# Optimization experiments

Hardware: AMD Instinct MI355X
Metric: run time of the kernel (lower is better)

## Reference

```python
import jax, jax.numpy as jnp
import numpy as np
from jax import lax

N, C_IN, DIMS, NW, T, H, W = 8, 64, 64, 8, 16, 64, 64
BN_EPS = 1e-5


def setup_inputs() -> dict:
    key = jax.random.key(0)
    ks = jax.random.split(key, 10)
    # kaiming-ish scales
    w_scale = (2.0 / (C_IN * 27)) ** 0.5
    return {
        "x": jax.random.normal(ks[0], (N, C_IN, T, H, W), dtype=jnp.float32),
        "weights": jax.random.normal(ks[1], (NW, DIMS, C_IN, 3, 3, 3), dtype=jnp.float32) * w_scale,
        "biases": jax.random.normal(ks[2], (NW, DIMS), dtype=jnp.float32),
        "se_w1": jax.random.normal(ks[3], (16, C_IN, 5, 5), dtype=jnp.float32) * (2.0 / (C_IN * 25)) ** 0.5,
        "se_b1": jnp.zeros((16,), dtype=jnp.float32),
        "se_w2": jax.random.normal(ks[4], (32, 16, 5, 5), dtype=jnp.float32) * (2.0 / (16 * 25)) ** 0.5,
        "se_b2": jnp.zeros((32,), dtype=jnp.float32),
        "lin_w": jax.random.normal(ks[5], (NW, 32), dtype=jnp.float32) * (1.0 / 32) ** 0.5,
        "lin_b": jnp.zeros((NW,), dtype=jnp.float32),
        "bn_gamma": jnp.ones((DIMS,), dtype=jnp.float32),
        "bn_beta": jnp.zeros((DIMS,), dtype=jnp.float32),
        "epochs_num": 15,
    }


def _forward(x, weights, biases, se_w1, se_b1, se_w2, se_b2, lin_w, lin_b, bn_gamma, bn_beta, epochs_num):
    tau = 30.0 - 2.9 * epochs_num if epochs_num < 10 else 1.0
    # std over temporal axis (torch.std -> unbiased, ddof=1): [n, c, h, w]
    std_x = jnp.std(x, axis=2, ddof=1)
    # squeeze-expand attention branch
    dn2d = ("NCHW", "OIHW", "NCHW")
    h1 = lax.conv_general_dilated(std_x, se_w1, (1, 1), "VALID", dimension_numbers=dn2d)
    h1 = jax.nn.relu(h1 + se_b1[None, :, None, None])
    h2 = lax.conv_general_dilated(h1, se_w2, (1, 1), "VALID", dimension_numbers=dn2d)
    h2 = jax.nn.relu(h2 + se_b2[None, :, None, None])
    pooled = jnp.max(h2, axis=(2, 3))                      # [n, 32]
    logits = pooled @ lin_w.T + lin_b                       # [n, num_weights]
    phi = jax.nn.softmax(logits / tau, axis=1)
    # per-sample dynamic kernels / biases
    dyn_w = jnp.einsum("bn,ncidhw->bcidhw", phi, weights)   # [n, dims, c_in, 3,3,3]
    dyn_b = phi @ biases                                    # [n, dims]
    # grouped conv3d (groups = n) == per-sample conv3d via vmap
    dn3d = ("NCDHW", "OIDHW", "NCDHW")
    def one_conv(xi, wi):
        return lax.conv_general_dilated(xi[None], wi, (1, 1, 1), "SAME", dimension_numbers=dn3d)[0]
    y = jax.vmap(one_conv)(x, dyn_w)                        # [n, dims, t, h, w]
    y = y + dyn_b[:, :, None, None, None]
    # BatchNorm3d (training mode, batch stats, biased var)
    mean = jnp.mean(y, axis=(0, 2, 3, 4))
    var = jnp.var(y, axis=(0, 2, 3, 4))
    b = lambda v: v[None, :, None, None, None]
    y = (y - b(mean)) * b(bn_gamma) * lax.rsqrt(b(var) + BN_EPS) + b(bn_beta)
    return jax.nn.relu(y)


def reference(x, weights, biases, se_w1, se_b1, se_w2, se_b2, lin_w, lin_b, bn_gamma, bn_beta, epochs_num):
    return _forward(x, weights, biases, se_w1, se_b1, se_w2, se_b2, lin_w, lin_b, bn_gamma, bn_beta, epochs_num)
```

## Files before the change

### kernel.cpp

```cpp
#include <hip/hip_runtime.h>
#include <hip/hip_bf16.h>
#include <math.h>

#define N_   8
#define CIN_ 64
#define DIMS_ 64
#define NW_  8
#define T_   16
#define H_   64
#define W_   64
#define HW_  (H_ * W_)
#define THW_ (T_ * HW_)

typedef short bf16x8 __attribute__((ext_vector_type(8)));
typedef float f32x16 __attribute__((ext_vector_type(16)));

__device__ __forceinline__ unsigned short f2bf(float f) {
    union { float f; unsigned u; } a; a.f = f;
    unsigned r = a.u + 0x7fffu + ((a.u >> 16) & 1u);
    return (unsigned short)(r >> 16);
}

#define CS8_ 8
#define HS8_ (66 * CS8_)
#define TS8_ (10 * HS8_)
#define XSH_ (3 * TS8_)
#define WLH_ (28 * 64 * 8)

__host__ __device__ constexpr int OXc(int tap) {
    int tt = tap > 26 ? 26 : tap;
    return (tt / 9) * TS8_ + ((tt % 9) / 3) * HS8_ + ((tt % 3) - 1) * CS8_;
}

__global__ __launch_bounds__(512) void stdxb_kernel(
    const float* __restrict__ x, float* __restrict__ std_x,
    unsigned short* __restrict__ xb)
{
    __shared__ unsigned short xsl[16 * 64 * 8];
    const int h = blockIdx.x, c8 = blockIdx.y, n = blockIdx.z;
    const int tid = threadIdx.x;
    const int c = tid >> 6, w = tid & 63;
    const int cin = c8 * 8 + c;
    const float* px = x + (((size_t)(n * 64 + cin)) << 16) + (h << 6) + w;
    float s = 0.f, s2 = 0.f;
#pragma unroll
    for (int t = 0; t < T_; ++t) {
        float v = px[t * HW_];
        s += v;
        s2 += v * v;
        xsl[(t << 9) + (w << 3) + c] = f2bf(v);
    }
    float var = (s2 - s * s * (1.0f / 16.0f)) * (1.0f / 15.0f);
    std_x[(((size_t)(n * 64 + cin)) << 12) + (h << 6) + w] = sqrtf(fmaxf(var, 0.f));
    __syncthreads();
    const int4* src = (const int4*)xsl;
    int4* dst = (int4*)(xb + ((size_t)((n * 8 + c8) * 16) << 12) * 8);
#pragma unroll
    for (int k = 0; k < 2; ++k) {
        int j = tid + (k << 9);
        int t = j >> 6, ww = j & 63;
        dst[((t << 6) + h) * 64 + ww] = src[j];
    }
}

__global__ void wtrans(const float* __restrict__ w1, const float* __restrict__ w2,
                       float* __restrict__ w1t, float* __restrict__ w2t) {
    int i = blockIdx.x * 256 + threadIdx.x;
    if (i < 25600) {
        int k = i / 1600, c = (i / 25) % 64, tap = i % 25;
        w1t[(c * 25 + tap) * 16 + k] = w1[i];
    } else if (i < 38400) {
        int j = i - 25600;
        int o = j / 400, c = (j / 25) % 16, tap = j % 25;
        w2t[(c * 25 + tap) * 32 + o] = w2[j];
    }
}

__global__ __launch_bounds__(256) void se_conv1c(const float* __restrict__ std_x,
        const float* __restrict__ w1t, const float* __restrict__ b1, float* __restrict__ h1) {
    __shared__ float red[3][64][8];
    const int n = blockIdx.y, ks = blockIdx.z * 8;
    const int iq = threadIdx.x & 63, cq = threadIdx.x >> 6;
    const int ij = blockIdx.x * 64 + iq;
    float acc[8];
#pragma unroll
    for (int q = 0; q < 8; ++q) acc[q] = 0.f;
    if (ij < 3600) {
        int i = ij / 60, j = ij - i * 60;
        const float* xn = std_x + (size_t)n * CIN_ * HW_ + i * W_ + j;
        for (int c = cq * 16; c < cq * 16 + 16; ++c) {
            const float* xc = xn + c * HW_;
            float xv[25];
#pragma unroll
            for (int u = 0; u < 5; ++u)
#pragma unroll
                for (int v = 0; v < 5; ++v) xv[u * 5 + v] = xc[u * W_ + v];
            const float* wc = w1t + c * 400 + ks;
#pragma unroll
            for (int tap = 0; tap < 25; ++tap)
#pragma unroll
                for (int q = 0; q < 8; ++q)
                    acc[q] = fmaf(xv[tap], wc[tap * 16 + q], acc[q]);
        }
    }
    if (cq > 0) {
#pragma unroll
        for (int q = 0; q < 8; ++q) red[cq - 1][iq][q] = acc[q];
    }
    __syncthreads();
    if (cq == 0 && ij < 3600) {
#pragma unroll
        for (int q = 0; q < 8; ++q) {
            float a = acc[q] + red[0][iq][q] + red[1][iq][q] + red[2][iq][q] + b1[ks + q];
            h1[((size_t)(n * 16 + ks + q)) * 3600 + ij] = fmaxf(a, 0.f);
        }
    }
}

__global__ __launch_bounds__(256) void se_conv2c(const float* __restrict__ h1,
        const float* __restrict__ w2t, const float* __restrict__ b2,
        unsigned* __restrict__ pooled) {
    __shared__ float red[3][64][8];
    const int n = blockIdx.y, os = blockIdx.z * 8;
    const int iq = threadIdx.x & 63, cq = threadIdx.x >> 6;
    const int ij = blockIdx.x * 64 + iq;
    const int i = ij / 56, j = ij - i * 56;
    float acc[8];
#pragma unroll
    for (int q = 0; q < 8; ++q) acc[q] = 0.f;
    const float* xn = h1 + (size_t)n * 16 * 3600 + i * 60 + j;
    for (int c = cq * 4; c < cq * 4 + 4; ++c) {
        const float* xc = xn + c * 3600;
        float xv[25];
#pragma unroll
        for (int u = 0; u < 5; ++u)
#pragma unroll
            for (int v = 0; v < 5; ++v) xv[u * 5 + v] = xc[u * 60 + v];
        const float* wc = w2t + c * 800 + os;
#pragma unroll
        for (int tap = 0; tap < 25; ++tap)
#pragma unroll
            for (int q = 0; q < 8; ++q)
                acc[q] = fmaf(xv[tap], wc[tap * 32 + q], acc[q]);
    }
    if (cq > 0) {
#pragma unroll
        for (int q = 0; q < 8; ++q) red[cq - 1][iq][q] = acc[q];
    }
    __syncthreads();
    if (cq == 0) {
#pragma unroll
        for (int q = 0; q < 8; ++q) {
            float a = fmaxf(acc[q] + red[0][iq][q] + red[1][iq][q] + red[2][iq][q] + b2[os + q], 0.f);
#pragma unroll
            for (int m = 1; m < 64; m <<= 1) a = fmaxf(a, __shfl_xor(a, m, 64));
            if (iq == 0) atomicMax(&pooled[n * 32 + os + q], __float_as_uint(a));
        }
    }
}

__global__ void se_head(const float* __restrict__ pooled, const float* __restrict__ lin_w,
                        const float* __restrict__ lin_b, const float* __restrict__ biases,
                        const int* __restrict__ epochs, float* __restrict__ phi,
                        float* __restrict__ dyn_b) {
    __shared__ float sphi[NW_][NW_];
    int tid = threadIdx.x;
    int e = epochs[0];
    float tau = (e < 10) ? (30.0f - 2.9f * (float)e) : 1.0f;
    if (tid < 64) {
        int b = tid >> 3, m = tid & 7;
        float acc = lin_b[m];
        for (int k = 0; k < 32; ++k) acc += pooled[b * 32 + k] * lin_w[m * 32 + k];
        sphi[b][m] = acc / tau;
    }
    __syncthreads();
    if (tid < 8) {
        int b = tid;
        float mx = sphi[b][0];
#pragma unroll
        for (int m = 1; m < 8; ++m) mx = fmaxf(mx, sphi[b][m]);
        float ex[8], s = 0.f;
#pragma unroll
        for (int m = 0; m < 8; ++m) { ex[m] = expf(sphi[b][m] - mx); s += ex[m]; }
        float inv = 1.0f / s;
#pragma unroll
        for (int m = 0; m < 8; ++m) { sphi[b][m] = ex[m] * inv; phi[b * 8 + m] = ex[m] * inv; }
    }
    __syncthreads();
    for (int idx = tid; idx < NW_ * DIMS_; idx += blockDim.x) {
        int b = idx >> 6, d = idx & 63;
        float acc = 0.f;
#pragma unroll
        for (int m = 0; m < 8; ++m) acc += sphi[b][m] * biases[m * DIMS_ + d];
        dyn_b[idx] = acc;
    }
}

__global__ void dyn_w_bf16b(const float* __restrict__ weights, const float* __restrict__ phi,
                            unsigned short* __restrict__ wtb2) {
    int g = blockIdx.x * 256 + threadIdx.x;
    int b = blockIdx.y;
    int c8 = g / 14336, r = g - c8 * 14336;
    int tap = r >> 9, co = (r >> 3) & 63, ci = r & 7;
    int cin = c8 * 8 + ci;
    unsigned short v = 0;
    if (tap < 27) {
        size_t src = ((size_t)(co * 64) + cin) * 27 + tap;
        float acc = 0.f;
#pragma unroll
        for (int m = 0; m < 8; ++m)
            acc += phi[b * 8 + m] * weights[(size_t)m * (64 * 64 * 27) + src];
        v = f2bf(acc);
    }
    wtb2[(size_t)b * 114688 + g] = v;
}

__global__ __launch_bounds__(512, 4) void conv3d_mfma3(
    const unsigned short* __restrict__ xb,
    const unsigned short* __restrict__ wtb2,
    const float* __restrict__ dynb,
    float* __restrict__ y,
    float* __restrict__ sums)
{
    __shared__ __align__(16) unsigned short xs[XSH_];
    __shared__ __align__(16) unsigned short wl[WLH_];
    __shared__ float bnred[128];

    const int hb = blockIdx.x, t = blockIdx.y, n = blockIdx.z;
    const int tid = threadIdx.x;
    const int lane = tid & 63, wid = tid >> 6;
    const int lane31 = lane & 31, tau = lane >> 5;
    const int hbase = hb * 8;

    for (int i = tid; i < XSH_ / 8; i += 512)
        *(int4*)&xs[i * 8] = (int4){0, 0, 0, 0};
    if (tid < 128) bnred[tid] = 0.f;

    const unsigned short* xnb = xb + ((size_t)(n * 8) << 16) * 8;
    const unsigned short* wnb = wtb2 + (size_t)n * 114688;

    f32x16 acc[2][2];
#pragma unroll
    for (int ci = 0; ci < 2; ++ci)
#pragma unroll
        for (int s = 0; s < 2; ++s)
            acc[ci][s] = (f32x16)(0.f);

    const int aBase = (tau * 64 + lane31) * 8;
    const int bsp0 = wid * HS8_ + (1 + lane31) * CS8_;
    const int bsp1 = bsp0 + 32 * CS8_;

    for (int c8 = 0; c8 < 8; ++c8) {
        __syncthreads();
#pragma unroll
        for (int k = 0; k < 4; ++k) {
            int r = wid + (k << 3);
            if (r < 30) {
                int tp = (r >= 20) ? 2 : (r >= 10 ? 1 : 0);
                int hp = r - tp * 10;
                int gt = t + tp - 1, gh = hbase + hp - 1;
                if (((unsigned)gt < 16u) && ((unsigned)gh < 64u)) {
                    const unsigned short* gp = xnb + (size_t)(((c8 * 16 + gt) * 64 + gh) * 64 + lane) * 8;
                    const unsigned short* lp = &xs[tp * TS8_ + hp * HS8_ + CS8_];
                    __builtin_amdgcn_global_load_lds(
                        (const __attribute__((address_space(1))) void*)gp,
                        (__attribute__((address_space(3))) void*)lp, 16, 0, 0);
                }
            }
        }
#pragma unroll
        for (int k = 0; k < 4; ++k) {
            int tp = wid + (k << 3);
            if (tp < 28) {
                const unsigned short* gp = wnb + (size_t)(c8 * 14336 + tp * 512 + lane * 8);
                const unsigned short* lp = &wl[tp * 512];
                __builtin_amdgcn_global_load_lds(
                    (const __attribute__((address_space(1))) void*)gp,
                    (__attribute__((address_space(3))) void*)lp, 16, 0, 0);
            }
        }
        __syncthreads();

#pragma unroll
        for (int p = 0; p < 14; ++p) {
            const int xo = tau ? OXc(2 * p + 1) : OXc(2 * p);
            bf16x8 a0 = *(const bf16x8*)&wl[p * 1024 + aBase];
            bf16x8 a1 = *(const bf16x8*)&wl[p * 1024 + aBase + 256];
            bf16x8 b0 = *(const bf16x8*)&xs[bsp0 + xo];
            bf16x8 b1 = *(const bf16x8*)&xs[bsp1 + xo];
            acc[0][0] = __builtin_amdgcn_mfma_f32_32x32x16_bf16(a0, b0, acc[0][0], 0, 0, 0);
            acc[0][1] = __builtin_amdgcn_mfma_f32_32x32x16_bf16(a0, b1, acc[0][1], 0, 0, 0);
            acc[1][0] = __builtin_amdgcn_mfma_f32_32x32x16_bf16(a1, b0, acc[1][0], 0, 0, 0);
            acc[1][1] = __builtin_amdgcn_mfma_f32_32x32x16_bf16(a1, b1, acc[1][1], 0, 0, 0);
        }
    }

    const float* db = dynb + n * DIMS_;
    const size_t ybase = (((size_t)n * DIMS_) << 16) + ((size_t)t << 12) + ((size_t)(hbase + wid) << 6);
#pragma unroll
    for (int ci = 0; ci < 2; ++ci) {
#pragma unroll
        for (int r = 0; r < 16; ++r) {
            const int co = 32 * ci + (r & 3) + 8 * (r >> 2) + 4 * tau;
            const float bco = db[co];
            float z0 = acc[ci][0][r] + bco;
            float z1 = acc[ci][1][r] + bco;
            y[ybase + ((size_t)co << 16) + lane31]      = z0;
            y[ybase + ((size_t)co << 16) + 32 + lane31] = z1;
            float ps = z0 + z1, ps2 = z0 * z0 + z1 * z1;
#pragma unroll
            for (int m = 1; m < 32; m <<= 1) {
                ps += __shfl_xor(ps, m, 64);
                ps2 += __shfl_xor(ps2, m, 64);
            }
            if (lane31 == 0) {
                atomicAdd(&bnred[co], ps);
                atomicAdd(&bnred[64 + co], ps2);
            }
        }
    }
    __syncthreads();
    if (tid < 128) atomicAdd(&sums[tid], bnred[tid]);
}

__global__ void bn_norm4(const float* __restrict__ sums, const float* __restrict__ gamma,
                         const float* __restrict__ beta, float* __restrict__ y) {
    size_t idx = (size_t)blockIdx.x * 256 + threadIdx.x;
    int c = (int)((idx >> 14) & 63);
    const float cnt = (float)(N_ * THW_);
    float mean = sums[c] / cnt;
    float var = sums[64 + c] / cnt - mean * mean;
    float sc = gamma[c] * rsqrtf(var + 1e-5f);
    float sh = beta[c] - mean * sc;
    float4 v = ((float4*)y)[idx];
    v.x = fmaxf(fmaf(v.x, sc, sh), 0.f);
    v.y = fmaxf(fmaf(v.y, sc, sh), 0.f);
    v.z = fmaxf(fmaf(v.z, sc, sh), 0.f);
    v.w = fmaxf(fmaf(v.w, sc, sh), 0.f);
    ((float4*)y)[idx] = v;
}

extern "C" void kernel_launch(void* const* d_in, const int* in_sizes, int n_in,
                              void* d_out, int out_size, void* d_ws, size_t ws_size,
                              hipStream_t stream) {
    const float* x       = (const float*)d_in[0];
    const float* weights = (const float*)d_in[1];
    const float* biases  = (const float*)d_in[2];
    const float* se_w1   = (const float*)d_in[3];
    const float* se_b1   = (const float*)d_in[4];
    const float* se_w2   = (const float*)d_in[5];
    const float* se_b2   = (const float*)d_in[6];
    const float* lin_w   = (const float*)d_in[7];
    const float* lin_b   = (const float*)d_in[8];
    const float* gamma   = (const float*)d_in[9];
    const float* beta    = (const float*)d_in[10];
    const int*   epochs  = (const int*)d_in[11];

    float* out = (float*)d_out;
    float* ws = (float*)d_ws;

    const size_t STD_OFF  = 0;
    const size_t H1_OFF   = STD_OFF + 2097152;
    const size_t SUMS_OFF = H1_OFF + 460800;
    const size_t POOL_OFF = SUMS_OFF + 128;
    const size_t PHI_OFF  = POOL_OFF + 256;
    const size_t DYNB_OFF = PHI_OFF + 64;
    const size_t WTB_OFF  = DYNB_OFF + 512;
    const size_t W1T_OFF  = WTB_OFF + 458752;
    const size_t W2T_OFF  = W1T_OFF + 25600;
    const size_t XB_OFF   = W2T_OFF + 12800;

    float* std_x  = ws + STD_OFF;
    float* h1     = ws + H1_OFF;
    float* sums   = ws + SUMS_OFF;
    float* pooled = ws + POOL_OFF;
    float* phi    = ws + PHI_OFF;
    float* dynb   = ws + DYNB_OFF;
    unsigned short* wtb2 = (unsigned short*)(ws + WTB_OFF);
    float* w1t    = ws + W1T_OFF;
    float* w2t    = ws + W2T_OFF;
    unsigned short* xb = (unsigned short*)(ws + XB_OFF);

    hipMemsetAsync(sums, 0, (128 + 256) * sizeof(float), stream);

    stdxb_kernel<<<dim3(64, 8, 8), 512, 0, stream>>>(x, std_x, xb);
    wtrans<<<150, 256, 0, stream>>>(se_w1, se_w2, w1t, w2t);

    se_conv1c<<<dim3(57, 8, 2), 256, 0, stream>>>(std_x, w1t, se_b1, h1);
    se_conv2c<<<dim3(49, 8, 4), 256, 0, stream>>>(h1, w2t, se_b2, (unsigned*)pooled);
    se_head<<<1, 64, 0, stream>>>(pooled, lin_w, lin_b, biases, epochs, phi, dynb);

    dyn_w_bf16b<<<dim3(448, 8), 256, 0, stream>>>(weights, phi, wtb2);

    conv3d_mfma3<<<dim3(8, 16, 8), 512, 0, stream>>>(xb, wtb2, dynb, out, sums);

    bn_norm4<<<32768, 256, 0, stream>>>(sums, gamma, beta, out);
}
```

Before: 408.5 us.

## Double-buffer conv3d LDS staging and restructure dynamic-weight and BN kernels

The conv3d kernel now uses dynamic shared memory with two x/w buffers and prefetches the next channel-group chunk with async global-to-LDS loads while the current chunk feeds the MFMAs. Waits use explicit vmcnt counts, with out-of-range loads redirected to a junk LDS slot so the count stays fixed. The dynamic-weight kernel now reads each base weight once and writes all 8 per-sample outputs, relying on a memset to zero the padding tap. BN normalization switches to a grid-stride loop over fewer blocks. Doubled LDS may lower occupancy, and the launch-bounds min-blocks hint is dropped.

```diff
diff --git a/kernel.cpp b/kernel.cpp
--- a/kernel.cpp
+++ b/kernel.cpp
@@ -24,8 +24,11 @@
 #define CS8_ 8
 #define HS8_ (66 * CS8_)
 #define TS8_ (10 * HS8_)
-#define XSH_ (3 * TS8_)
-#define WLH_ (28 * 64 * 8)
+#define XBUF_ (3 * TS8_)
+#define WBUF_ (28 * 64 * 8)
+#define JUNK_OFF_ (2 * XBUF_ + 2 * WBUF_)
+#define BNRED_OFF_ (JUNK_OFF_ + 512)
+#define DLS_BYTES_ (BNRED_OFF_ * 2 + 128 * 4)
 
 __host__ __device__ constexpr int OXc(int tap) {
     int tt = tap > 26 ? 26 : tap;
@@ -196,48 +199,82 @@
     }
 }
 
-__global__ void dyn_w_bf16b(const float* __restrict__ weights, const float* __restrict__ phi,
-                            unsigned short* __restrict__ wtb2) {
-    int g = blockIdx.x * 256 + threadIdx.x;
-    int b = blockIdx.y;
-    int c8 = g / 14336, r = g - c8 * 14336;
-    int tap = r >> 9, co = (r >> 3) & 63, ci = r & 7;
-    int cin = c8 * 8 + ci;
-    unsigned short v = 0;
-    if (tap < 27) {
-        size_t src = ((size_t)(co * 64) + cin) * 27 + tap;
+__global__ void dyn_w_all(const float* __restrict__ weights, const float* __restrict__ phi,
+                          unsigned short* __restrict__ wtb2) {
+    __shared__ float sphi[64];
+    int tid = threadIdx.x;
+    if (tid < 64) sphi[tid] = phi[tid];
+    __syncthreads();
+    int f = blockIdx.x * 256 + tid;
+    if (f >= 110592) return;
+    int tap = f % 27, cin = (f / 27) & 63, co = f / 1728;
+    float wv[8];
+#pragma unroll
+    for (int m = 0; m < 8; ++m) wv[m] = weights[(size_t)m * 110592 + f];
+    size_t dbase = (size_t)(cin >> 3) * 14336 + tap * 512 + co * 8 + (cin & 7);
+#pragma unroll
+    for (int b = 0; b < 8; ++b) {
         float acc = 0.f;
 #pragma unroll
-        for (int m = 0; m < 8; ++m)
-            acc += phi[b * 8 + m] * weights[(size_t)m * (64 * 64 * 27) + src];
-        v = f2bf(acc);
-    }
-    wtb2[(size_t)b * 114688 + g] = v;
-}
-
-__global__ __launch_bounds__(512, 4) void conv3d_mfma3(
+        for (int m = 0; m < 8; ++m) acc += sphi[b * 8 + m] * wv[m];
+        wtb2[(size_t)b * 114688 + dbase] = f2bf(acc);
+    }
+}
+
+extern __shared__ unsigned short dls[];
+
+__global__ __launch_bounds__(512) void conv3d_mfma4(
     const unsigned short* __restrict__ xb,
     const unsigned short* __restrict__ wtb2,
     const float* __restrict__ dynb,
     float* __restrict__ y,
     float* __restrict__ sums)
 {
-    __shared__ __align__(16) unsigned short xs[XSH_];
-    __shared__ __align__(16) unsigned short wl[WLH_];
-    __shared__ float bnred[128];
-
     const int hb = blockIdx.x, t = blockIdx.y, n = blockIdx.z;
     const int tid = threadIdx.x;
     const int lane = tid & 63, wid = tid >> 6;
     const int lane31 = lane & 31, tau = lane >> 5;
     const int hbase = hb * 8;
 
-    for (int i = tid; i < XSH_ / 8; i += 512)
-        *(int4*)&xs[i * 8] = (int4){0, 0, 0, 0};
+    unsigned short* junk = dls + JUNK_OFF_;
+    float* bnred = (float*)(dls + BNRED_OFF_);
+
+    for (int i = tid; i < (2 * XBUF_) / 8; i += 512)
+        *(int4*)&dls[i * 8] = (int4){0, 0, 0, 0};
     if (tid < 128) bnred[tid] = 0.f;
-
-    const unsigned short* xnb = xb + ((size_t)(n * 8) << 16) * 8;
+    __syncthreads();
+
+    const unsigned short* xnb = xb + (size_t)n * 4194304;
     const unsigned short* wnb = wtb2 + (size_t)n * 114688;
+
+    auto STAGE = [&](int c8, int pb) {
+        unsigned short* xbuf = dls + pb * XBUF_;
+        unsigned short* wbuf = dls + 2 * XBUF_ + pb * WBUF_;
+#pragma unroll
+        for (int k = 0; k < 4; ++k) {
+            int tp = wid + (k << 3);
+            bool ok = tp < 28;
+            const unsigned short* gp = wnb + ((size_t)c8 * 14336 + (ok ? tp * 512 : 0) + lane * 8);
+            unsigned short* lp = ok ? (wbuf + tp * 512) : junk;
+            __builtin_amdgcn_global_load_lds(
+                (const __attribute__((address_space(1))) void*)gp,
+                (__attribute__((address_space(3))) void*)lp, 16, 0, 0);
+        }
+#pragma unroll
+        for (int k = 0; k < 4; ++k) {
+            int r = wid + (k << 3);
+            int tp = (r >= 20) ? 2 : (r >= 10 ? 1 : 0);
+            int hp = r - tp * 10;
+            int gt = t + tp - 1, gh = hbase + hp - 1;
+            bool ok = (r < 30) && ((unsigned)gt < 16u) && ((unsigned)gh < 64u);
+            const unsigned short* gp = xnb +
+                (ok ? (size_t)(((c8 * 16 + gt) * 64 + gh) * 64 + lane) * 8 : (size_t)lane * 8);
+            unsigned short* lp = ok ? (xbuf + tp * TS8_ + hp * HS8_ + CS8_) : junk;
+            __builtin_amdgcn_global_load_lds(
+                (const __attribute__((address_space(1))) void*)gp,
+                (__attribute__((address_space(3))) void*)lp, 16, 0, 0);
+        }
+    };
 
     f32x16 acc[2][2];
 #pragma unroll
@@ -250,49 +287,33 @@
     const int bsp0 = wid * HS8_ + (1 + lane31) * CS8_;
     const int bsp1 = bsp0 + 32 * CS8_;
 
+    STAGE(0, 0);
+
     for (int c8 = 0; c8 < 8; ++c8) {
-        __syncthreads();
-#pragma unroll
-        for (int k = 0; k < 4; ++k) {
-            int r = wid + (k << 3);
-            if (r < 30) {
-                int tp = (r >= 20) ? 2 : (r >= 10 ? 1 : 0);
-                int hp = r - tp * 10;
-                int gt = t + tp - 1, gh = hbase + hp - 1;
-                if (((unsigned)gt < 16u) && ((unsigned)gh < 64u)) {
-                    const unsigned short* gp = xnb + (size_t)(((c8 * 16 + gt) * 64 + gh) * 64 + lane) * 8;
-                    const unsigned short* lp = &xs[tp * TS8_ + hp * HS8_ + CS8_];
-                    __builtin_amdgcn_global_load_lds(
-                        (const __attribute__((address_space(1))) void*)gp,
-                        (__attribute__((address_space(3))) void*)lp, 16, 0, 0);
-                }
-            }
-        }
-#pragma unroll
-        for (int k = 0; k < 4; ++k) {
-            int tp = wid + (k << 3);
-            if (tp < 28) {
-                const unsigned short* gp = wnb + (size_t)(c8 * 14336 + tp * 512 + lane * 8);
-                const unsigned short* lp = &wl[tp * 512];
-                __builtin_amdgcn_global_load_lds(
-                    (const __attribute__((address_space(1))) void*)gp,
-                    (__attribute__((address_space(3))) void*)lp, 16, 0, 0);
-            }
-        }
-        __syncthreads();
-
+        if (c8 < 7) {
+            STAGE(c8 + 1, (c8 + 1) & 1);
+            asm volatile("s_waitcnt vmcnt(8)" ::: "memory");
+        } else {
+            asm volatile("s_waitcnt vmcnt(0)" ::: "memory");
+        }
+        __builtin_amdgcn_s_barrier();
+        __builtin_amdgcn_sched_barrier(0);
+
+        const unsigned short* xsb = dls + (c8 & 1) * XBUF_;
+        const unsigned short* wlb = dls + 2 * XBUF_ + (c8 & 1) * WBUF_;
 #pragma unroll
         for (int p = 0; p < 14; ++p) {
             const int xo = tau ? OXc(2 * p + 1) : OXc(2 * p);
-            bf16x8 a0 = *(const bf16x8*)&wl[p * 1024 + aBase];
-            bf16x8 a1 = *(const bf16x8*)&wl[p * 1024 + aBase + 256];
-            bf16x8 b0 = *(const bf16x8*)&xs[bsp0 + xo];
-            bf16x8 b1 = *(const bf16x8*)&xs[bsp1 + xo];
+            bf16x8 a0 = *(const bf16x8*)&wlb[p * 1024 + aBase];
+            bf16x8 a1 = *(const bf16x8*)&wlb[p * 1024 + aBase + 256];
+            bf16x8 b0 = *(const bf16x8*)&xsb[bsp0 + xo];
+            bf16x8 b1 = *(const bf16x8*)&xsb[bsp1 + xo];
             acc[0][0] = __builtin_amdgcn_mfma_f32_32x32x16_bf16(a0, b0, acc[0][0], 0, 0, 0);
             acc[0][1] = __builtin_amdgcn_mfma_f32_32x32x16_bf16(a0, b1, acc[0][1], 0, 0, 0);
             acc[1][0] = __builtin_amdgcn_mfma_f32_32x32x16_bf16(a1, b0, acc[1][0], 0, 0, 0);
             acc[1][1] = __builtin_amdgcn_mfma_f32_32x32x16_bf16(a1, b1, acc[1][1], 0, 0, 0);
         }
+        __builtin_amdgcn_s_barrier();
     }
 
     const float* db = dynb + n * DIMS_;
@@ -325,19 +346,21 @@
 
 __global__ void bn_norm4(const float* __restrict__ sums, const float* __restrict__ gamma,
                          const float* __restrict__ beta, float* __restrict__ y) {
-    size_t idx = (size_t)blockIdx.x * 256 + threadIdx.x;
-    int c = (int)((idx >> 14) & 63);
     const float cnt = (float)(N_ * THW_);
-    float mean = sums[c] / cnt;
-    float var = sums[64 + c] / cnt - mean * mean;
-    float sc = gamma[c] * rsqrtf(var + 1e-5f);
-    float sh = beta[c] - mean * sc;
-    float4 v = ((float4*)y)[idx];
-    v.x = fmaxf(fmaf(v.x, sc, sh), 0.f);
-    v.y = fmaxf(fmaf(v.y, sc, sh), 0.f);
-    v.z = fmaxf(fmaf(v.z, sc, sh), 0.f);
-    v.w = fmaxf(fmaf(v.w, sc, sh), 0.f);
-    ((float4*)y)[idx] = v;
+    for (size_t idx = (size_t)blockIdx.x * 256 + threadIdx.x; idx < 8388608;
+         idx += (size_t)4096 * 256) {
+        int c = (int)((idx >> 14) & 63);
+        float mean = sums[c] / cnt;
+        float var = sums[64 + c] / cnt - mean * mean;
+        float sc = gamma[c] * rsqrtf(var + 1e-5f);
+        float sh = beta[c] - mean * sc;
+        float4 v = ((float4*)y)[idx];
+        v.x = fmaxf(fmaf(v.x, sc, sh), 0.f);
+        v.y = fmaxf(fmaf(v.y, sc, sh), 0.f);
+        v.z = fmaxf(fmaf(v.z, sc, sh), 0.f);
+        v.w = fmaxf(fmaf(v.w, sc, sh), 0.f);
+        ((float4*)y)[idx] = v;
+    }
 }
 
 extern "C" void kernel_launch(void* const* d_in, const int* in_sizes, int n_in,
@@ -381,7 +404,11 @@
     float* w2t    = ws + W2T_OFF;
     unsigned short* xb = (unsigned short*)(ws + XB_OFF);
 
+    hipFuncSetAttribute((const void*)conv3d_mfma4,
+                        hipFuncAttributeMaxDynamicSharedMemorySize, DLS_BYTES_);
+
     hipMemsetAsync(sums, 0, (128 + 256) * sizeof(float), stream);
+    hipMemsetAsync(wtb2, 0, (size_t)8 * 114688 * sizeof(unsigned short), stream);
 
     stdxb_kernel<<<dim3(64, 8, 8), 512, 0, stream>>>(x, std_x, xb);
     wtrans<<<150, 256, 0, stream>>>(se_w1, se_w2, w1t, w2t);
@@ -390,9 +417,9 @@
     se_conv2c<<<dim3(49, 8, 4), 256, 0, stream>>>(h1, w2t, se_b2, (unsigned*)pooled);
     se_head<<<1, 64, 0, stream>>>(pooled, lin_w, lin_b, biases, epochs, phi, dynb);
 
-    dyn_w_bf16b<<<dim3(448, 8), 256, 0, stream>>>(weights, phi, wtb2);
-
-    conv3d_mfma3<<<dim3(8, 16, 8), 512, 0, stream>>>(xb, wtb2, dynb, out, sums);
-
-    bn_norm4<<<32768, 256, 0, stream>>>(sums, gamma, beta, out);
-}
+    dyn_w_all<<<432, 256, 0, stream>>>(weights, phi, wtb2);
+
+    conv3d_mfma4<<<dim3(8, 16, 8), 512, DLS_BYTES_, stream>>>(xb, wtb2, dynb, out, sums);
+
+    bn_norm4<<<4096, 256, 0, stream>>>(sums, gamma, beta, out);
+}
```

After: 402.1 us. No clear change (-1.6%).
